# Optimization experiments

Measured on AMD Instinct MI355X. Metric: run time of the kernel, lower is better.

Reference implementation:

```python
import jax, jax.numpy as jnp
import numpy as np

B, N, F, K = 4, 512, 128, 32
GAMMA = 10.0          # RBF width parameter
CUTOFF = 5.0          # RBF center range [0, CUTOFF]
LOG2 = 0.6931471805599453
EPS = 1e-12           # keeps sqrt grad finite on the (masked-out) diagonal


def ssp(x):
    # shifted softplus: ln(0.5*e^x + 0.5) = softplus(x) - ln 2
    return jax.nn.softplus(x) - LOG2


def setup_inputs() -> dict:
    key = jax.random.key(0)
    ks = jax.random.split(key, 8)
    coordinates = jax.random.normal(ks[0], (B, N, 3), dtype=jnp.float32) * 3.0
    atom_emb = jax.random.normal(ks[1], (B, N, F), dtype=jnp.float32)
    rbf_centers = jnp.linspace(0.0, CUTOFF, K, dtype=jnp.float32)
    # cfconv filter-generator dense layers
    w1 = jax.random.normal(ks[2], (K, F), dtype=jnp.float32) / np.float32(np.sqrt(K))
    b1 = jnp.zeros((F,), dtype=jnp.float32)
    w2 = jax.random.normal(ks[3], (F, F), dtype=jnp.float32) / np.float32(np.sqrt(F))
    b2 = jnp.zeros((F,), dtype=jnp.float32)
    # self.W linear (nn.Linear stores weight as [out, in])
    Ww = jax.random.normal(ks[4], (F, F), dtype=jnp.float32) / np.float32(np.sqrt(F))
    Wb = jnp.zeros((F,), dtype=jnp.float32)
    return {"coordinates": coordinates, "atom_emb": atom_emb,
            "rbf_centers": rbf_centers, "w1": w1, "b1": b1,
            "w2": w2, "b2": b2, "Ww": Ww, "Wb": Wb}


def reference(coordinates, atom_emb, rbf_centers, w1, b1, w2, b2, Ww, Wb):
    n = coordinates.shape[-2]
    # pairwise distances [B, N, N]
    diff = coordinates[:, :, None, :] - coordinates[:, None, :, :]
    d = jnp.sqrt(jnp.sum(diff * diff, axis=-1) + EPS)
    # Gaussian RBF expansion [B, N, N, K]
    rbf = jnp.exp(-GAMMA * (d[..., None] - rbf_centers) ** 2)
    # filter generator: Dense -> SSP -> Dense -> SSP  => W [B, N, N, F]
    Wf = ssp(jnp.einsum('bnmk,kf->bnmf', rbf, w1) + b1)
    Wf = ssp(jnp.einsum('bnmf,fg->bnmg', Wf, w2) + b2)
    # zero the diagonal (no self-interaction)
    mask = (1.0 - jnp.eye(n, dtype=Wf.dtype))[None, :, :, None]
    Wf = Wf * mask
    # x = self.W(atom_emb)
    x = atom_emb @ Ww.T + Wb
    # per-channel weighted neighbor aggregation
    x = jnp.einsum('bnmf,bmf->bnf', Wf, x)
    return atom_emb + x
```

## Files before the change

kernel.cpp:

```cpp
#include <hip/hip_runtime.h>
#include <hip/hip_bf16.h>

#define B_ 4
#define N_ 512
#define F_ 128
#define K_ 32
#define TD 1024
#define DMAX 6.5f
#define XWB (B_ * N_ / 2)

typedef __attribute__((ext_vector_type(4))) float f32x4;

__device__ __forceinline__ unsigned cvt_pk_bf16(float a, float b) {
  unsigned r;
  asm("v_cvt_pk_bf16_f32 %0, %1, %2" : "=v"(r) : "v"(a), "v"(b));
  return r;
}
__device__ __forceinline__ unsigned short f2bf1(float a) {
  return (unsigned short)cvt_pk_bf16(a, a);
}
__device__ __forceinline__ float exp2_hw(float x) {
  float r; asm("v_exp_f32 %0, %1" : "=v"(r) : "v"(x)); return r;
}
__device__ __forceinline__ float log2_hw(float x) {
  float r; asm("v_log_f32 %0, %1" : "=v"(r) : "v"(x)); return r;
}
__device__ __forceinline__ float lo16f(unsigned w) {
  return __builtin_bit_cast(float, w << 16);
}
__device__ __forceinline__ float hi16f(unsigned w) {
  return __builtin_bit_cast(float, w & 0xffff0000u);
}

__device__ __forceinline__ float sspb(float u) {
  float e = exp2_hw(__builtin_fabsf(u) * -1.4426950408889634f);
  float l = log2_hw(fmaf(e, 0.5f, 0.5f));
  return fmaf(l, 0.6931471805599453f, fmaxf(u, 0.f));
}

__launch_bounds__(256)
__global__ void prep_kernel(const float* __restrict__ emb, const float* __restrict__ Ww,
                            const float* __restrict__ Wb,
                            const float* __restrict__ w1, const float* __restrict__ b1,
                            const float* __restrict__ w2, const float* __restrict__ b2,
                            unsigned short* __restrict__ xbf, unsigned* __restrict__ tab2) {
  __shared__ float erow[2][F_];
  __shared__ float rbf_s[2][K_];
  __shared__ float h1s[2][F_];
  __shared__ float fs[2][F_];

  if (blockIdx.x < XWB) {
    const int r0 = blockIdx.x * 2;
    const int half = threadIdx.x >> 7, f = threadIdx.x & 127;
    erow[half][f] = emb[(r0 + half) * F_ + f];
    __syncthreads();
    const float4* w4 = (const float4*)(Ww + f * F_);
    const float* er = erow[half];
    float acc = 0.f;
#pragma unroll 8
    for (int g4 = 0; g4 < F_ / 4; ++g4) {
      float4 wv = w4[g4];
      acc = fmaf(er[g4 * 4 + 0], wv.x, acc);
      acc = fmaf(er[g4 * 4 + 1], wv.y, acc);
      acc = fmaf(er[g4 * 4 + 2], wv.z, acc);
      acc = fmaf(er[g4 * 4 + 3], wv.w, acc);
    }
    xbf[(r0 + half) * F_ + f] = f2bf1(acc + Wb[f]);
  } else {
    const int i = blockIdx.x - XWB;
    const int sl = threadIdx.x >> 7, f = threadIdx.x & 127;
    const float d = (float)(i + sl) * (DMAX / (float)(TD - 1));
    if (f < K_) {
      float t = d - (float)f * (5.0f / 31.0f);
      rbf_s[sl][f] = exp2_hw(t * t * -14.426950408889634f);
    }
    __syncthreads();
    float a1 = b1[f];
#pragma unroll 8
    for (int k = 0; k < K_; ++k) a1 = fmaf(rbf_s[sl][k], w1[k * F_ + f], a1);
    h1s[sl][f] = sspb(a1);
    __syncthreads();
    float a2 = b2[f];
#pragma unroll 8
    for (int g = 0; g < F_; ++g) a2 = fmaf(h1s[sl][g], w2[g * F_ + f], a2);
    fs[sl][f] = sspb(a2);
    __syncthreads();
    if (sl == 0)
      tab2[i * F_ + f] = cvt_pk_bf16(fs[0][f], fs[1][f] - fs[0][f]);
  }
}

__launch_bounds__(256, 8)
__global__ void agg_kernel(const float* __restrict__ coords, const float* __restrict__ emb,
                           const unsigned short* __restrict__ xbf,
                           const unsigned* __restrict__ tab2,
                           float* __restrict__ out) {
  __shared__ float tvr[N_];
  __shared__ float ctv[N_];
  __shared__ unsigned cid[N_];
  __shared__ unsigned cnt_s;
  __shared__ float part[16][F_ + 4];

  const int blk = blockIdx.x;
  const int b = blk >> 9, n = blk & 511;
  const int tid = threadIdx.x;
  const int lane = tid & 63;

  const float cx = coords[(b * N_ + n) * 3 + 0];
  const float cy = coords[(b * N_ + n) * 3 + 1];
  const float cz = coords[(b * N_ + n) * 3 + 2];

  for (int m = tid; m < N_; m += 256) {
    const float* cm = coords + (b * N_ + m) * 3;
    float dx = cm[0] - cx, dy = cm[1] - cy, dz = cm[2] - cz;
    float d = sqrtf(fmaf(dx, dx, fmaf(dy, dy, fmaf(dz, dz, 1e-12f))));
    float t = d * ((float)(TD - 1) / DMAX);
    tvr[m] = fminf(t, (float)(TD - 2) + 0.999f);
  }
  __syncthreads();

  if (tid < 64) {
    unsigned base = 0;
#pragma unroll 1
    for (int chunk = 0; chunk < N_ / 64; ++chunk) {
      int m = chunk * 64 + lane;
      float tv = tvr[m];
      bool keep = tv < 1022.0f;
      unsigned long long msk = __ballot(keep);
      unsigned pos = base + (unsigned)__popcll(msk & ((1ull << lane) - 1ull));
      if (keep) { ctv[pos] = tv; cid[pos] = (unsigned)m; }
      base += (unsigned)__popcll(msk);
    }
    if (lane == 0) cnt_s = base;
  }
  __syncthreads();
  const int cnt = (int)cnt_s;

  const int mg = tid >> 4;
  const int f0 = (tid & 15) * 8;
  const unsigned short* xp = xbf + b * N_ * F_ + f0;

  f32x4 acc0 = {0.f, 0.f, 0.f, 0.f};
  f32x4 acc1 = {0.f, 0.f, 0.f, 0.f};

#define PAIR_STEP(TV, M, SGN)                                               \
  {                                                                         \
    float tv = (TV);                                                        \
    int i = (int)tv;                                                        \
    float fr = tv - (float)i;                                               \
    const uint4* tp = (const uint4*)(tab2 + i * F_ + f0);                   \
    uint4 ta = tp[0], tb = tp[1];                                           \
    uint4 xv = *(const uint4*)(xp + (M) * F_);                              \
    float v;                                                                \
    v = fmaf(fr, hi16f(ta.x), lo16f(ta.x));                                 \
    acc0[0] = fmaf(SGN v, lo16f(xv.x), acc0[0]);                            \
    v = fmaf(fr, hi16f(ta.y), lo16f(ta.y));                                 \
    acc0[1] = fmaf(SGN v, hi16f(xv.x), acc0[1]);                            \
    v = fmaf(fr, hi16f(ta.z), lo16f(ta.z));                                 \
    acc0[2] = fmaf(SGN v, lo16f(xv.y), acc0[2]);                            \
    v = fmaf(fr, hi16f(ta.w), lo16f(ta.w));                                 \
    acc0[3] = fmaf(SGN v, hi16f(xv.y), acc0[3]);                            \
    v = fmaf(fr, hi16f(tb.x), lo16f(tb.x));                                 \
    acc1[0] = fmaf(SGN v, lo16f(xv.z), acc1[0]);                            \
    v = fmaf(fr, hi16f(tb.y), lo16f(tb.y));                                 \
    acc1[1] = fmaf(SGN v, hi16f(xv.z), acc1[1]);                            \
    v = fmaf(fr, hi16f(tb.z), lo16f(tb.z));                                 \
    acc1[2] = fmaf(SGN v, lo16f(xv.w), acc1[2]);                            \
    v = fmaf(fr, hi16f(tb.w), lo16f(tb.w));                                 \
    acc1[3] = fmaf(SGN v, hi16f(xv.w), acc1[3]);                            \
  }

#pragma unroll 1
  for (int k = mg; k < cnt; k += 16) {
    PAIR_STEP(ctv[k], cid[k], +)
  }

  if (mg == 0) {
    PAIR_STEP(tvr[n], (unsigned)n, -)
  }
#undef PAIR_STEP

  *(f32x4*)&part[mg][f0] = acc0;
  *(f32x4*)&part[mg][f0 + 4] = acc1;
  __syncthreads();

  if (tid < F_) {
    float s = 0.f;
#pragma unroll
    for (int g = 0; g < 16; ++g) s += part[g][tid];
    int o = (b * N_ + n) * F_ + tid;
    out[o] = emb[o] + s;
  }
}

extern "C" void kernel_launch(void* const* d_in, const int* in_sizes, int n_in,
                              void* d_out, int out_size, void* d_ws, size_t ws_size,
                              hipStream_t stream) {
  const float* coords = (const float*)d_in[0];
  const float* emb    = (const float*)d_in[1];
  const float* w1 = (const float*)d_in[3];
  const float* b1 = (const float*)d_in[4];
  const float* w2 = (const float*)d_in[5];
  const float* b2 = (const float*)d_in[6];
  const float* Ww = (const float*)d_in[7];
  const float* Wb = (const float*)d_in[8];
  float* out = (float*)d_out;

  unsigned short* xbf = (unsigned short*)d_ws;
  unsigned* tab2 = (unsigned*)(xbf + B_ * N_ * F_);

  hipLaunchKernelGGL(prep_kernel, dim3(XWB + TD - 1), dim3(256), 0, stream,
                     emb, Ww, Wb, w1, b1, w2, b2, xbf, tab2);
  hipLaunchKernelGGL(agg_kernel, dim3(B_ * N_), dim3(256), 0, stream,
                     coords, emb, xbf, tab2, out);
}
```

Before: 46.74 us.

## Halve filter table, tighten neighbor cutoff, exclude self, and prefetch next pair

Shrinks the distance lookup table from 1024 to 512 entries, which halves the prep work spent generating filter rows. The kept-neighbor threshold drops from about 6.5 to 6.0 distance units. The diagonal is now excluded during compaction instead of being subtracted afterwards. The aggregation loop is software-pipelined so the next pair's table and x loads are issued before the current pair's FMAs, using a padded sentinel entry to avoid bounds branches. The trade-off is coarser interpolation and a cutoff-based truncation that assumes the filter is negligible beyond 6.0, which may cost accuracy.

```diff
diff --git a/kernel.cpp b/kernel.cpp
--- a/kernel.cpp
+++ b/kernel.cpp
@@ -5,7 +5,7 @@
 #define N_ 512
 #define F_ 128
 #define K_ 32
-#define TD 1024
+#define TD 512
 #define DMAX 6.5f
 #define XWB (B_ * N_ / 2)
 
@@ -96,8 +96,8 @@
                            const unsigned* __restrict__ tab2,
                            float* __restrict__ out) {
   __shared__ float tvr[N_];
-  __shared__ float ctv[N_];
-  __shared__ unsigned cid[N_];
+  __shared__ float ctv[N_ + 1];
+  __shared__ unsigned cid[N_ + 1];
   __shared__ unsigned cnt_s;
   __shared__ float part[16][F_ + 4];
 
@@ -114,24 +114,28 @@
     const float* cm = coords + (b * N_ + m) * 3;
     float dx = cm[0] - cx, dy = cm[1] - cy, dz = cm[2] - cz;
     float d = sqrtf(fmaf(dx, dx, fmaf(dy, dy, fmaf(dz, dz, 1e-12f))));
-    float t = d * ((float)(TD - 1) / DMAX);
-    tvr[m] = fminf(t, (float)(TD - 2) + 0.999f);
+    tvr[m] = d * ((float)(TD - 1) / DMAX);
   }
   __syncthreads();
 
+  const float TKEEP = 6.0f * ((float)(TD - 1) / DMAX);
   if (tid < 64) {
     unsigned base = 0;
 #pragma unroll 1
     for (int chunk = 0; chunk < N_ / 64; ++chunk) {
       int m = chunk * 64 + lane;
       float tv = tvr[m];
-      bool keep = tv < 1022.0f;
+      bool keep = (tv < TKEEP) && (m != n);
       unsigned long long msk = __ballot(keep);
       unsigned pos = base + (unsigned)__popcll(msk & ((1ull << lane) - 1ull));
       if (keep) { ctv[pos] = tv; cid[pos] = (unsigned)m; }
       base += (unsigned)__popcll(msk);
     }
-    if (lane == 0) cnt_s = base;
+    if (lane == 0) {
+      cnt_s = base;
+      ctv[base] = 0.f;
+      cid[base] = 0u;
+    }
   }
   __syncthreads();
   const int cnt = (int)cnt_s;
@@ -143,42 +147,48 @@
   f32x4 acc0 = {0.f, 0.f, 0.f, 0.f};
   f32x4 acc1 = {0.f, 0.f, 0.f, 0.f};
 
-#define PAIR_STEP(TV, M, SGN)                                               \
-  {                                                                         \
-    float tv = (TV);                                                        \
-    int i = (int)tv;                                                        \
-    float fr = tv - (float)i;                                               \
-    const uint4* tp = (const uint4*)(tab2 + i * F_ + f0);                   \
-    uint4 ta = tp[0], tb = tp[1];                                           \
-    uint4 xv = *(const uint4*)(xp + (M) * F_);                              \
-    float v;                                                                \
-    v = fmaf(fr, hi16f(ta.x), lo16f(ta.x));                                 \
-    acc0[0] = fmaf(SGN v, lo16f(xv.x), acc0[0]);                            \
-    v = fmaf(fr, hi16f(ta.y), lo16f(ta.y));                                 \
-    acc0[1] = fmaf(SGN v, hi16f(xv.x), acc0[1]);                            \
-    v = fmaf(fr, hi16f(ta.z), lo16f(ta.z));                                 \
-    acc0[2] = fmaf(SGN v, lo16f(xv.y), acc0[2]);                            \
-    v = fmaf(fr, hi16f(ta.w), lo16f(ta.w));                                 \
-    acc0[3] = fmaf(SGN v, hi16f(xv.y), acc0[3]);                            \
-    v = fmaf(fr, hi16f(tb.x), lo16f(tb.x));                                 \
-    acc1[0] = fmaf(SGN v, lo16f(xv.z), acc1[0]);                            \
-    v = fmaf(fr, hi16f(tb.y), lo16f(tb.y));                                 \
-    acc1[1] = fmaf(SGN v, hi16f(xv.z), acc1[1]);                            \
-    v = fmaf(fr, hi16f(tb.z), lo16f(tb.z));                                 \
-    acc1[2] = fmaf(SGN v, lo16f(xv.w), acc1[2]);                            \
-    v = fmaf(fr, hi16f(tb.w), lo16f(tb.w));                                 \
-    acc1[3] = fmaf(SGN v, hi16f(xv.w), acc1[3]);                            \
-  }
+  int k = mg;
+  int idx = (k < cnt) ? k : cnt;
+  float tv = ctv[idx];
+  unsigned id = cid[idx];
+  int ii = (int)tv;
+  float fr = tv - (float)ii;
+  const uint4* tp = (const uint4*)(tab2 + ii * F_ + f0);
+  uint4 ta = tp[0], tb = tp[1];
+  uint4 xv = *(const uint4*)(xp + id * F_);
 
 #pragma unroll 1
-  for (int k = mg; k < cnt; k += 16) {
-    PAIR_STEP(ctv[k], cid[k], +)
-  }
-
-  if (mg == 0) {
-    PAIR_STEP(tvr[n], (unsigned)n, -)
-  }
-#undef PAIR_STEP
+  while (k < cnt) {
+    int kn = k + 16;
+    int idxn = (kn < cnt) ? kn : cnt;
+    float tvn = ctv[idxn];
+    unsigned idn = cid[idxn];
+    int iin = (int)tvn;
+    float frn = tvn - (float)iin;
+    const uint4* tpn = (const uint4*)(tab2 + iin * F_ + f0);
+    uint4 tan = tpn[0], tbn = tpn[1];
+    uint4 xvn = *(const uint4*)(xp + idn * F_);
+
+    float v;
+    v = fmaf(fr, hi16f(ta.x), lo16f(ta.x));
+    acc0[0] = fmaf(v, lo16f(xv.x), acc0[0]);
+    v = fmaf(fr, hi16f(ta.y), lo16f(ta.y));
+    acc0[1] = fmaf(v, hi16f(xv.x), acc0[1]);
+    v = fmaf(fr, hi16f(ta.z), lo16f(ta.z));
+    acc0[2] = fmaf(v, lo16f(xv.y), acc0[2]);
+    v = fmaf(fr, hi16f(ta.w), lo16f(ta.w));
+    acc0[3] = fmaf(v, hi16f(xv.y), acc0[3]);
+    v = fmaf(fr, hi16f(tb.x), lo16f(tb.x));
+    acc1[0] = fmaf(v, lo16f(xv.z), acc1[0]);
+    v = fmaf(fr, hi16f(tb.y), lo16f(tb.y));
+    acc1[1] = fmaf(v, hi16f(xv.z), acc1[1]);
+    v = fmaf(fr, hi16f(tb.z), lo16f(tb.z));
+    acc1[2] = fmaf(v, lo16f(xv.w), acc1[2]);
+    v = fmaf(fr, hi16f(tb.w), lo16f(tb.w));
+    acc1[3] = fmaf(v, hi16f(xv.w), acc1[3]);
+
+    k = kn; fr = frn; ta = tan; tb = tbn; xv = xvn;
+  }
 
   *(f32x4*)&part[mg][f0] = acc0;
   *(f32x4*)&part[mg][f0 + 4] = acc1;
```

New measurement: 41.36 us. 11.5% less time.

## Replace interpolated filter table with finer nearest-neighbor bf16 table and prefetch loop

Applied to the files above, without the earlier changes.

Doubles the distance table resolution and switches from linear interpolation (value plus delta pairs) to nearest-entry lookup in a single bf16 table. This halves table bytes per pair and drops the interpolation FMAs. Each neighbor is packed as a table index and atom id in one word, and the diagonal is excluded at compaction instead of subtracted afterwards. The aggregation loop is software-pipelined to load two pairs ahead, with sentinel entries padding the end. The trade-off is accuracy from nearest-neighbor quantization, a doubled prep table cost, and a lower occupancy bound.

```diff
diff --git a/kernel.cpp b/kernel.cpp
--- a/kernel.cpp
+++ b/kernel.cpp
@@ -5,9 +5,10 @@
 #define N_ 512
 #define F_ 128
 #define K_ 32
-#define TD 1024
+#define TD 2048
 #define DMAX 6.5f
 #define XWB (B_ * N_ / 2)
+#define TKEEPI 1890
 
 typedef __attribute__((ext_vector_type(4))) float f32x4;
 
@@ -43,11 +44,11 @@
                             const float* __restrict__ Wb,
                             const float* __restrict__ w1, const float* __restrict__ b1,
                             const float* __restrict__ w2, const float* __restrict__ b2,
-                            unsigned short* __restrict__ xbf, unsigned* __restrict__ tab2) {
+                            unsigned short* __restrict__ xbf,
+                            unsigned short* __restrict__ tabn) {
   __shared__ float erow[2][F_];
   __shared__ float rbf_s[2][K_];
   __shared__ float h1s[2][F_];
-  __shared__ float fs[2][F_];
 
   if (blockIdx.x < XWB) {
     const int r0 = blockIdx.x * 2;
@@ -67,9 +68,10 @@
     }
     xbf[(r0 + half) * F_ + f] = f2bf1(acc + Wb[f]);
   } else {
-    const int i = blockIdx.x - XWB;
+    const int j = blockIdx.x - XWB;
     const int sl = threadIdx.x >> 7, f = threadIdx.x & 127;
-    const float d = (float)(i + sl) * (DMAX / (float)(TD - 1));
+    const int i = 2 * j + sl;
+    const float d = (float)i * (DMAX / (float)(TD - 1));
     if (f < K_) {
       float t = d - (float)f * (5.0f / 31.0f);
       rbf_s[sl][f] = exp2_hw(t * t * -14.426950408889634f);
@@ -83,21 +85,17 @@
     float a2 = b2[f];
 #pragma unroll 8
     for (int g = 0; g < F_; ++g) a2 = fmaf(h1s[sl][g], w2[g * F_ + f], a2);
-    fs[sl][f] = sspb(a2);
-    __syncthreads();
-    if (sl == 0)
-      tab2[i * F_ + f] = cvt_pk_bf16(fs[0][f], fs[1][f] - fs[0][f]);
-  }
-}
-
-__launch_bounds__(256, 8)
+    tabn[i * F_ + f] = f2bf1(sspb(a2));
+  }
+}
+
+__launch_bounds__(256, 6)
 __global__ void agg_kernel(const float* __restrict__ coords, const float* __restrict__ emb,
                            const unsigned short* __restrict__ xbf,
-                           const unsigned* __restrict__ tab2,
+                           const unsigned short* __restrict__ tabn,
                            float* __restrict__ out) {
-  __shared__ float tvr[N_];
-  __shared__ float ctv[N_];
-  __shared__ unsigned cid[N_];
+  __shared__ unsigned tci[N_];
+  __shared__ unsigned cidx[N_ + 80];
   __shared__ unsigned cnt_s;
   __shared__ float part[16][F_ + 4];
 
@@ -110,12 +108,13 @@
   const float cy = coords[(b * N_ + n) * 3 + 1];
   const float cz = coords[(b * N_ + n) * 3 + 2];
 
+  const float SC = (float)(TD - 1) / DMAX;
   for (int m = tid; m < N_; m += 256) {
     const float* cm = coords + (b * N_ + m) * 3;
     float dx = cm[0] - cx, dy = cm[1] - cy, dz = cm[2] - cz;
     float d = sqrtf(fmaf(dx, dx, fmaf(dy, dy, fmaf(dz, dz, 1e-12f))));
-    float t = d * ((float)(TD - 1) / DMAX);
-    tvr[m] = fminf(t, (float)(TD - 2) + 0.999f);
+    int ti = (int)fminf(fmaf(d, SC, 0.5f), (float)(TD - 1));
+    tci[m] = ((unsigned)ti << 16) | (unsigned)m;
   }
   __syncthreads();
 
@@ -124,13 +123,14 @@
 #pragma unroll 1
     for (int chunk = 0; chunk < N_ / 64; ++chunk) {
       int m = chunk * 64 + lane;
-      float tv = tvr[m];
-      bool keep = tv < 1022.0f;
+      unsigned v = tci[m];
+      bool keep = ((v >> 16) < TKEEPI) && (m != n);
       unsigned long long msk = __ballot(keep);
       unsigned pos = base + (unsigned)__popcll(msk & ((1ull << lane) - 1ull));
-      if (keep) { ctv[pos] = tv; cid[pos] = (unsigned)m; }
+      if (keep) cidx[pos] = v;
       base += (unsigned)__popcll(msk);
     }
+    cidx[base + lane] = ((unsigned)(TD - 1)) << 16;
     if (lane == 0) cnt_s = base;
   }
   __syncthreads();
@@ -139,46 +139,46 @@
   const int mg = tid >> 4;
   const int f0 = (tid & 15) * 8;
   const unsigned short* xp = xbf + b * N_ * F_ + f0;
+  const unsigned short* tp = tabn + f0;
 
   f32x4 acc0 = {0.f, 0.f, 0.f, 0.f};
   f32x4 acc1 = {0.f, 0.f, 0.f, 0.f};
 
-#define PAIR_STEP(TV, M, SGN)                                               \
-  {                                                                         \
-    float tv = (TV);                                                        \
-    int i = (int)tv;                                                        \
-    float fr = tv - (float)i;                                               \
-    const uint4* tp = (const uint4*)(tab2 + i * F_ + f0);                   \
-    uint4 ta = tp[0], tb = tp[1];                                           \
-    uint4 xv = *(const uint4*)(xp + (M) * F_);                              \
-    float v;                                                                \
-    v = fmaf(fr, hi16f(ta.x), lo16f(ta.x));                                 \
-    acc0[0] = fmaf(SGN v, lo16f(xv.x), acc0[0]);                            \
-    v = fmaf(fr, hi16f(ta.y), lo16f(ta.y));                                 \
-    acc0[1] = fmaf(SGN v, hi16f(xv.x), acc0[1]);                            \
-    v = fmaf(fr, hi16f(ta.z), lo16f(ta.z));                                 \
-    acc0[2] = fmaf(SGN v, lo16f(xv.y), acc0[2]);                            \
-    v = fmaf(fr, hi16f(ta.w), lo16f(ta.w));                                 \
-    acc0[3] = fmaf(SGN v, hi16f(xv.y), acc0[3]);                            \
-    v = fmaf(fr, hi16f(tb.x), lo16f(tb.x));                                 \
-    acc1[0] = fmaf(SGN v, lo16f(xv.z), acc1[0]);                            \
-    v = fmaf(fr, hi16f(tb.y), lo16f(tb.y));                                 \
-    acc1[1] = fmaf(SGN v, hi16f(xv.z), acc1[1]);                            \
-    v = fmaf(fr, hi16f(tb.z), lo16f(tb.z));                                 \
-    acc1[2] = fmaf(SGN v, lo16f(xv.w), acc1[2]);                            \
-    v = fmaf(fr, hi16f(tb.w), lo16f(tb.w));                                 \
-    acc1[3] = fmaf(SGN v, hi16f(xv.w), acc1[3]);                            \
-  }
-
+#define LOADP(V, T, X)                                                       \
+  {                                                                          \
+    unsigned v_ = (V);                                                       \
+    T = *(const uint4*)(tp + (v_ >> 16) * F_);                               \
+    X = *(const uint4*)(xp + (v_ & 0xffffu) * F_);                           \
+  }
+#define MAC8(T, X)                                                           \
+  {                                                                          \
+    acc0[0] = fmaf(lo16f(T.x), lo16f(X.x), acc0[0]);                         \
+    acc0[1] = fmaf(hi16f(T.x), hi16f(X.x), acc0[1]);                         \
+    acc0[2] = fmaf(lo16f(T.y), lo16f(X.y), acc0[2]);                         \
+    acc0[3] = fmaf(hi16f(T.y), hi16f(X.y), acc0[3]);                         \
+    acc1[0] = fmaf(lo16f(T.z), lo16f(X.z), acc1[0]);                         \
+    acc1[1] = fmaf(hi16f(T.z), hi16f(X.z), acc1[1]);                         \
+    acc1[2] = fmaf(lo16f(T.w), lo16f(X.w), acc1[2]);                         \
+    acc1[3] = fmaf(hi16f(T.w), hi16f(X.w), acc1[3]);                         \
+  }
+
+  uint4 tA, xA, tB, xB;
+  LOADP(cidx[mg], tA, xA)
+  LOADP(cidx[mg + 16], tB, xB)
+  int k = mg;
 #pragma unroll 1
-  for (int k = mg; k < cnt; k += 16) {
-    PAIR_STEP(ctv[k], cid[k], +)
-  }
-
-  if (mg == 0) {
-    PAIR_STEP(tvr[n], (unsigned)n, -)
-  }
-#undef PAIR_STEP
+  while (k < cnt) {
+    int kn = k + 32;
+    uint4 tC, xC, tD, xD;
+    LOADP(cidx[kn], tC, xC)
+    LOADP(cidx[kn + 16], tD, xD)
+    MAC8(tA, xA)
+    MAC8(tB, xB)
+    k = kn;
+    tA = tC; xA = xC; tB = tD; xB = xD;
+  }
+#undef LOADP
+#undef MAC8
 
   *(f32x4*)&part[mg][f0] = acc0;
   *(f32x4*)&part[mg][f0 + 4] = acc1;
@@ -206,11 +206,11 @@
   const float* Wb = (const float*)d_in[8];
   float* out = (float*)d_out;
 
-  unsigned short* xbf = (unsigned short*)d_ws;
-  unsigned* tab2 = (unsigned*)(xbf + B_ * N_ * F_);
-
-  hipLaunchKernelGGL(prep_kernel, dim3(XWB + TD - 1), dim3(256), 0, stream,
-                     emb, Ww, Wb, w1, b1, w2, b2, xbf, tab2);
+  unsigned short* xbf  = (unsigned short*)d_ws;
+  unsigned short* tabn = xbf + B_ * N_ * F_;
+
+  hipLaunchKernelGGL(prep_kernel, dim3(XWB + TD / 2), dim3(256), 0, stream,
+                     emb, Ww, Wb, w1, b1, w2, b2, xbf, tabn);
   hipLaunchKernelGGL(agg_kernel, dim3(B_ * N_), dim3(256), 0, stream,
-                     coords, emb, xbf, tab2, out);
-}
+                     coords, emb, xbf, tabn, out);
+}
```

New measurement: 39.45 us. 1.18x faster.
